# Performance work log

Hardware: AMD Instinct MI355X
Metric: run time of the kernel (lower is better)

The kernel has to match this reference:

```python
import jax, jax.numpy as jnp
import numpy as np

N = 100000
E = 3200000
IN_C = 512
HID = 64
LOC = 64
GLOB = 64
OUT_C = 40
K = 10
ALPHA = 0.1


def setup_inputs() -> dict:
    key = jax.random.key(0)
    ks = jax.random.split(key, 10)
    batch_x = jax.random.normal(ks[0], (N, IN_C), dtype=jnp.float32)
    edge_index = jax.random.randint(ks[1], (2, E), 0, N, dtype=jnp.int32)
    glob_emb = jax.random.normal(ks[2], (N, GLOB), dtype=jnp.float32)
    # Linear params (Glorot-ish scale)
    W1 = jax.random.normal(ks[3], (IN_C, HID), dtype=jnp.float32) / np.sqrt(IN_C)
    b1 = jnp.zeros((HID,), dtype=jnp.float32)
    W2 = jax.random.normal(ks[4], (HID, LOC), dtype=jnp.float32) / np.sqrt(HID)
    b2 = jnp.zeros((LOC,), dtype=jnp.float32)
    # GPR-GNN PPR init coefficients: temp[k] = alpha*(1-alpha)^k, temp[K] = (1-alpha)^K
    temp_np = ALPHA * (1.0 - ALPHA) ** np.arange(K + 1)
    temp_np[-1] = (1.0 - ALPHA) ** K
    temp = jnp.asarray(temp_np, dtype=jnp.float32)
    Wl = jax.random.normal(ks[5], (LOC + GLOB, OUT_C), dtype=jnp.float32) / np.sqrt(LOC + GLOB)
    bl = jnp.zeros((OUT_C,), dtype=jnp.float32)
    return {"batch_x": batch_x, "edge_index": edge_index, "glob_emb": glob_emb,
            "W1": W1, "b1": b1, "W2": W2, "b2": b2, "temp": temp, "Wl": Wl, "bl": bl}


def _gcn_norm(edge_index, num_nodes):
    # add self loops (weight 1), symmetric normalization like PyG gcn_norm
    loops = jnp.arange(num_nodes, dtype=edge_index.dtype)
    row = jnp.concatenate([edge_index[0], loops])  # sources
    col = jnp.concatenate([edge_index[1], loops])  # targets
    w = jnp.ones(row.shape[0], dtype=jnp.float32)
    deg = jax.ops.segment_sum(w, col, num_segments=num_nodes)
    dinv = jnp.where(deg > 0, jax.lax.rsqrt(jnp.maximum(deg, 1.0)), 0.0)
    norm = dinv[row] * dinv[col]
    return row, col, norm


def reference(batch_x, edge_index, glob_emb, W1, b1, W2, b2, temp, Wl, bl):
    # eval mode: all dropouts are identity
    x = jax.nn.relu(batch_x @ W1 + b1)
    x = x @ W2 + b2  # [N, LOC]
    n = x.shape[0]
    row, col, norm = _gcn_norm(edge_index, n)
    hidden = x * temp[0]
    for k in range(K):
        # message: norm * x[src]; aggregate: scatter-add at target
        x = jax.ops.segment_sum(norm[:, None] * x[row], col, num_segments=n)
        hidden = hidden + temp[k + 1] * x
    emb = jnp.concatenate([hidden, glob_emb], axis=1)  # [N, LOC+GLOB]
    return emb @ Wl + bl
```

## Files before the change

### kernel.cpp

```cpp
#include <hip/hip_runtime.h>


typedef _Float16 half8 __attribute__((ext_vector_type(8)));


__global__ __launch_bounds__(256) void count_kernel(const int* __restrict__ edge,
                                                    int* __restrict__ counts, int E) {
  int e = blockIdx.x * 256 + threadIdx.x;
  if (e < E) atomicAdd(&counts[edge[E + e]], 1);
}

__global__ __launch_bounds__(256) void bucketA_kernel(const int* __restrict__ edge,
                                                      unsigned long long* __restrict__ barr,
                                                      int* __restrict__ bcnt,
                                                      int E, int cap) {
  __shared__ int lcnt[64];
  __shared__ int lbase[64];
  int t = threadIdx.x;
  if (t < 64) lcnt[t] = 0;
  __syncthreads();
  int e0 = blockIdx.x * 2048 + t;
  int rk[8];
  int bk[8];
  unsigned long long pk[8];
#pragma unroll
  for (int i = 0; i < 8; ++i) {
    int e = e0 + i * 256;
    int s = 0, c = 0;
    if (e < E) { s = edge[e]; c = edge[E + e]; }
    int b = c >> 11;
    bk[i] = b;
    pk[i] = ((unsigned long long)(unsigned)c << 32) | (unsigned)s;
    if (e < E) rk[i] = atomicAdd(&lcnt[b], 1);
    else rk[i] = -1;
  }
  __syncthreads();
  if (t < 64 && lcnt[t] > 0) lbase[t] = atomicAdd(&bcnt[t], lcnt[t]);
  __syncthreads();
#pragma unroll
  for (int i = 0; i < 8; ++i)
    if (rk[i] >= 0)
      barr[(size_t)bk[i] * cap + lbase[bk[i]] + rk[i]] = pk[i];
}

__global__ __launch_bounds__(256) void fillB_kernel(const unsigned long long* __restrict__ barr,
                                                    const int* __restrict__ bcnt,
                                                    const int* __restrict__ rowptr,
                                                    int* __restrict__ cursor,
                                                    int* __restrict__ srcoff,
                                                    int cap, int nb, int nbx, int cpb) {
  int i = blockIdx.x;
  int x = i & 7;
  int j = i >> 3;
  int bslot = j % nbx;
  int chunk = j / nbx;
  int b = x + 8 * bslot;
  if (b >= nb) return;
  int cnt = bcnt[b];
  int lo = (int)((long long)cnt * chunk / cpb);
  int hi = (int)((long long)cnt * (chunk + 1) / cpb);
  const unsigned long long* ep = barr + (size_t)b * cap;
  for (int e = lo + threadIdx.x; e < hi; e += 256) {
    unsigned long long pk = ep[e];
    int s = (int)(unsigned)pk;
    int c = (int)(pk >> 32);
    int p = rowptr[c] + atomicAdd(&cursor[c], 1);
    srcoff[p] = s * 128;
  }
}

__global__ __launch_bounds__(256) void scanA_kernel(const int* __restrict__ counts,
                                                    int* __restrict__ incl,
                                                    int* __restrict__ partials, int Nn) {
  __shared__ int sbuf[256];
  int t = threadIdx.x;
  int base = blockIdx.x * 1024 + t * 4;
  int a0 = (base + 0 < Nn) ? counts[base + 0] : 0;
  int a1 = (base + 1 < Nn) ? counts[base + 1] : 0;
  int a2 = (base + 2 < Nn) ? counts[base + 2] : 0;
  int a3 = (base + 3 < Nn) ? counts[base + 3] : 0;
  int tot = a0 + a1 + a2 + a3;
  sbuf[t] = tot;
  __syncthreads();
  for (int off = 1; off < 256; off <<= 1) {
    int v = (t >= off) ? sbuf[t - off] : 0;
    __syncthreads();
    sbuf[t] += v;
    __syncthreads();
  }
  int excl = sbuf[t] - tot;
  if (base + 0 < Nn) incl[base + 0] = excl + a0;
  if (base + 1 < Nn) incl[base + 1] = excl + a0 + a1;
  if (base + 2 < Nn) incl[base + 2] = excl + a0 + a1 + a2;
  if (base + 3 < Nn) incl[base + 3] = excl + tot;
  if (t == 255) partials[blockIdx.x] = sbuf[255];
}

__global__ void scanB_kernel(const int* __restrict__ partials,
                             int* __restrict__ chunkoff, int B) {
  __shared__ int sbuf[256];
  int t = threadIdx.x;
  int v = (t < B) ? partials[t] : 0;
  sbuf[t] = v;
  __syncthreads();
  for (int off = 1; off < 256; off <<= 1) {
    int u = (t >= off) ? sbuf[t - off] : 0;
    __syncthreads();
    sbuf[t] += u;
    __syncthreads();
  }
  chunkoff[t] = sbuf[t] - v;
}

__global__ __launch_bounds__(256) void finalize_scan_kernel(const int* __restrict__ incl,
                                                            const int* __restrict__ chunkoff,
                                                            int* __restrict__ rowptr, int Nn) {
  int i = blockIdx.x * 256 + threadIdx.x;
  if (i < Nn) rowptr[i + 1] = incl[i] + chunkoff[i >> 10];
  if (i == 0) rowptr[0] = 0;
}

__global__ __launch_bounds__(256) void dinv_kernel(const int* __restrict__ counts,
                                                   float* __restrict__ dinv, int Nn) {
  int i = blockIdx.x * 256 + threadIdx.x;
  if (i < Nn) dinv[i] = rsqrtf((float)(counts[i] + 1));
}


__global__ __launch_bounds__(256) void mlp1_kernel(const float* __restrict__ X,
                                                   const float* __restrict__ W1,
                                                   const float* __restrict__ b1,
                                                   float* __restrict__ H, int Nn) {
  __shared__ float sXT[64][68];
  __shared__ float sW[64][68];
  int t = threadIdx.x;
  int m0 = blockIdx.x * 64;
  int tx = t & 15, ty = t >> 4;
  float acc[4][4];
#pragma unroll
  for (int i = 0; i < 4; ++i)
#pragma unroll
    for (int j = 0; j < 4; ++j) acc[i][j] = 0.f;

  for (int k0 = 0; k0 < 512; k0 += 64) {
#pragma unroll
    for (int i = 0; i < 4; ++i) {
      int lin = t + i * 256;
      int m = lin >> 4;
      int kq = lin & 15;
      int gr = m0 + m;
      float4 v = make_float4(0.f, 0.f, 0.f, 0.f);
      if (gr < Nn) v = *(const float4*)&X[(size_t)gr * 512 + k0 + kq * 4];
      sXT[kq * 4 + 0][m] = v.x;
      sXT[kq * 4 + 1][m] = v.y;
      sXT[kq * 4 + 2][m] = v.z;
      sXT[kq * 4 + 3][m] = v.w;
    }
#pragma unroll
    for (int i = 0; i < 4; ++i) {
      int lin = t + i * 256;
      int k = lin >> 4;
      int nq = lin & 15;
      float4 v = *(const float4*)&W1[(size_t)(k0 + k) * 64 + nq * 4];
      *(float4*)&sW[k][nq * 4] = v;
    }
    __syncthreads();
#pragma unroll 8
    for (int kk = 0; kk < 64; ++kk) {
      float4 a = *(const float4*)&sXT[kk][ty * 4];
      float4 b = *(const float4*)&sW[kk][tx * 4];
      float av[4] = {a.x, a.y, a.z, a.w};
      float bv[4] = {b.x, b.y, b.z, b.w};
#pragma unroll
      for (int i = 0; i < 4; ++i)
#pragma unroll
        for (int j = 0; j < 4; ++j) acc[i][j] += av[i] * bv[j];
    }
    __syncthreads();
  }
  float4 bb = *(const float4*)&b1[tx * 4];
  float bvv[4] = {bb.x, bb.y, bb.z, bb.w};
#pragma unroll
  for (int i = 0; i < 4; ++i) {
    int r = m0 + ty * 4 + i;
    if (r < Nn) {
      float4 o;
      o.x = fmaxf(acc[i][0] + bvv[0], 0.f);
      o.y = fmaxf(acc[i][1] + bvv[1], 0.f);
      o.z = fmaxf(acc[i][2] + bvv[2], 0.f);
      o.w = fmaxf(acc[i][3] + bvv[3], 0.f);
      *(float4*)&H[(size_t)r * 64 + tx * 4] = o;
    }
  }
}


__global__ void computeM_kernel(const float* __restrict__ W2, const float* __restrict__ Wl,
                                const float* __restrict__ b2, float* __restrict__ Mm,
                                float* __restrict__ cv) {
  int t = threadIdx.x;
  for (int idx = t; idx < 2560; idx += 256) {
    int k = idx / 40, o = idx - k * 40;
    float s = 0.f;
    for (int j = 0; j < 64; ++j) s += W2[k * 64 + j] * Wl[j * 40 + o];
    Mm[idx] = s;
  }
  if (t < 40) {
    float s = 0.f;
    for (int j = 0; j < 64; ++j) s += b2[j] * Wl[j * 40 + t];
    cv[t] = s;
  }
}

__global__ void zeropad_kernel(char* __restrict__ yA, char* __restrict__ yB, int Nn) {
  int t = threadIdx.x;
  ((_Float16*)(yA + (size_t)Nn * 128))[t] = (_Float16)0.f;
  ((_Float16*)(yB + (size_t)Nn * 128))[t] = (_Float16)0.f;
}


__global__ __launch_bounds__(256) void z0_kernel(const float* __restrict__ H,
                                                 const float* __restrict__ Mm,
                                                 const float* __restrict__ cv,
                                                 const float* __restrict__ dinv,
                                                 const float* __restrict__ temp,
                                                 char* __restrict__ y0,
                                                 float* __restrict__ hid, int Nn) {
  __shared__ float sM[2624];
  __shared__ float sc[40];
  int t = threadIdx.x;
  for (int i = t; i < 2560; i += 256) sM[i] = Mm[i];
  for (int i = 2560 + t; i < 2624; i += 256) sM[i] = 0.f;
  if (t < 40) sc[t] = cv[t];
  __syncthreads();
  int wid = t >> 6, lane = t & 63;
  int node = blockIdx.x * 4 + wid;
  if (node < Nn) {
    float h = H[(size_t)node * 64 + lane];
    float acc = (lane < 40) ? sc[lane] : 0.f;
#pragma unroll 8
    for (int k = 0; k < 64; ++k) acc += __shfl(h, k) * sM[k * 40 + lane];
    if (lane < 40) {
      float di = dinv[node];
      float y = di * acc;
      ((_Float16*)(y0 + (size_t)node * 128))[lane] = (_Float16)y;
      hid[(size_t)node * 40 + lane] = temp[0] * y;
    }
  }
}


__global__ __launch_bounds__(256) void prop_kernel(const char* __restrict__ yin,
                                                   char* __restrict__ yout,
                                                   float* __restrict__ hid,
                                                   const int* __restrict__ srcoff,
                                                   const int* __restrict__ rowptr,
                                                   const float* __restrict__ dinv,
                                                   const float* __restrict__ temp,
                                                   int kidx, int Nn) {
  __shared__ float red[4][60][8];
  int t = threadIdx.x, wid = t >> 6, lane = t & 63;
  int node = blockIdx.x * 4 + wid;
  int sub = lane / 5;
  int cl = lane - sub * 5;
  const int zoff = Nn * 128;
  float a0 = 0.f, a1 = 0.f, a2 = 0.f, a3 = 0.f, a4 = 0.f, a5 = 0.f, a6 = 0.f, a7 = 0.f;
  if (node < Nn) {
    int start = rowptr[node], end = rowptr[node + 1];
    int claneoff = cl << 4;
    for (int b0 = start; b0 < end; b0 += 60) {
      int j = b0 + lane;
      int moff = (lane < 60 && j < end) ? srcoff[j] : zoff;
#pragma unroll
      for (int tt = 0; tt < 5; ++tt) {
        int off = __shfl(moff, tt * 12 + sub);
        half8 v = *(const half8*)(yin + off + claneoff);
        a0 += (float)v[0]; a1 += (float)v[1]; a2 += (float)v[2]; a3 += (float)v[3];
        a4 += (float)v[4]; a5 += (float)v[5]; a6 += (float)v[6]; a7 += (float)v[7];
      }
    }
  }
  if (lane < 60) {
    red[wid][lane][0] = a0; red[wid][lane][1] = a1;
    red[wid][lane][2] = a2; red[wid][lane][3] = a3;
    red[wid][lane][4] = a4; red[wid][lane][5] = a5;
    red[wid][lane][6] = a6; red[wid][lane][7] = a7;
  }
  __syncthreads();
  if (node < Nn && lane < 5) {
    float s[8];
#pragma unroll
    for (int i = 0; i < 8; ++i) s[i] = 0.f;
#pragma unroll
    for (int g = 0; g < 12; ++g)
#pragma unroll
      for (int i = 0; i < 8; ++i) s[i] += red[wid][g * 5 + lane][i];
    float di = dinv[node];
    float m = di * di;
    half8 self = *(const half8*)(yin + (size_t)node * 128 + (lane << 4));
    float yn[8];
    half8 outv;
#pragma unroll
    for (int i = 0; i < 8; ++i) {
      yn[i] = m * (s[i] + (float)self[i]);
      outv[i] = (_Float16)yn[i];
    }
    *(half8*)(yout + (size_t)node * 128 + (lane << 4)) = outv;
    float tk = temp[kidx];
    float* hp = &hid[(size_t)node * 40 + lane * 8];
    float4 h0 = *(float4*)hp;
    float4 h1 = *(float4*)(hp + 4);
    h0.x += tk * yn[0]; h0.y += tk * yn[1]; h0.z += tk * yn[2]; h0.w += tk * yn[3];
    h1.x += tk * yn[4]; h1.y += tk * yn[5]; h1.z += tk * yn[6]; h1.w += tk * yn[7];
    *(float4*)hp = h0;
    *(float4*)(hp + 4) = h1;
  }
}


__global__ __launch_bounds__(256) void final_kernel(const float* __restrict__ glob,
                                                    const float* __restrict__ Wl,
                                                    const float* __restrict__ bl,
                                                    const float* __restrict__ hid,
                                                    const int* __restrict__ counts,
                                                    const float* __restrict__ dinv,
                                                    float* __restrict__ out, int Nn) {
  __shared__ float sW[2624];
  __shared__ float sb[40];
  int t = threadIdx.x;
  for (int i = t; i < 2560; i += 256) sW[i] = Wl[2560 + i];
  for (int i = 2560 + t; i < 2624; i += 256) sW[i] = 0.f;
  if (t < 40) sb[t] = bl[t];
  __syncthreads();
  int wid = t >> 6, lane = t & 63;
  int node = blockIdx.x * 4 + wid;
  if (node < Nn) {
    float g = glob[(size_t)node * 64 + lane];
    float acc = (lane < 40) ? sb[lane] : 0.f;
#pragma unroll 8
    for (int k = 0; k < 64; ++k) acc += __shfl(g, k) * sW[k * 40 + lane];
    if (lane < 40) {
      float sc = (float)(counts[node] + 1) * dinv[node];
      out[(size_t)node * 40 + lane] = sc * hid[(size_t)node * 40 + lane] + acc;
    }
  }
}


extern "C" void kernel_launch(void* const* d_in, const int* in_sizes, int n_in,
                              void* d_out, int out_size, void* d_ws, size_t ws_size,
                              hipStream_t stream) {
  const float* X    = (const float*)d_in[0];
  const int*   edge = (const int*)d_in[1];
  const float* glob = (const float*)d_in[2];
  const float* W1   = (const float*)d_in[3];
  const float* b1   = (const float*)d_in[4];
  const float* W2   = (const float*)d_in[5];
  const float* b2   = (const float*)d_in[6];
  const float* temp = (const float*)d_in[7];
  const float* Wl   = (const float*)d_in[8];
  const float* bl   = (const float*)d_in[9];
  float* out = (float*)d_out;

  int Nn = in_sizes[0] / 512;
  int E  = in_sizes[1] / 2;
  int Kk = in_sizes[7] - 1;

  char* p = (char*)d_ws;
  auto alloc = [&](size_t bytes) {
    char* r = p;
    p += (bytes + 255) & ~(size_t)255;
    return r;
  };
  int*   counts   = (int*)alloc((size_t)Nn * 4);
  int*   rowptr   = (int*)alloc((size_t)(Nn + 1) * 4);
  int*   incl     = (int*)alloc((size_t)Nn * 4);
  int*   partials = (int*)alloc(256 * 4);
  int*   chunkoff = (int*)alloc(256 * 4);
  int*   cursor   = (int*)alloc((size_t)Nn * 4);
  float* dinv     = (float*)alloc((size_t)Nn * 4);
  int*   srcoff   = (int*)alloc((size_t)E * 4);
  float* Hbuf     = (float*)alloc((size_t)Nn * 64 * 4);
  float* Mm       = (float*)alloc(2560 * 4);
  float* cv       = (float*)alloc(64 * 4);
  char*  yA       = (char*)alloc((size_t)(Nn + 1) * 128);
  char*  yB       = (char*)alloc((size_t)(Nn + 1) * 128);
  float* hid      = (float*)alloc((size_t)Nn * 40 * 4);

  int nb  = (Nn + 2047) >> 11;
  int nbx = (nb + 7) / 8;
  int cap = E / nb + E / (nb * 8) + 1024;
  unsigned long long* barr = (unsigned long long*)alloc((size_t)nb * cap * 8);
  int* bcnt = (int*)alloc(64 * 4);

  hipMemsetAsync(counts, 0, (size_t)Nn * 4, stream);
  hipMemsetAsync(cursor, 0, (size_t)Nn * 4, stream);
  hipMemsetAsync(bcnt, 0, 64 * 4, stream);

  count_kernel<<<(E + 255) / 256, 256, 0, stream>>>(edge, counts, E);
  bucketA_kernel<<<(E + 2047) / 2048, 256, 0, stream>>>(edge, barr, bcnt, E, cap);
  int B = (Nn + 1023) / 1024;
  scanA_kernel<<<B, 256, 0, stream>>>(counts, incl, partials, Nn);
  scanB_kernel<<<1, 256, 0, stream>>>(partials, chunkoff, B);
  finalize_scan_kernel<<<(Nn + 255) / 256, 256, 0, stream>>>(incl, chunkoff, rowptr, Nn);
  dinv_kernel<<<(Nn + 255) / 256, 256, 0, stream>>>(counts, dinv, Nn);
  int cpb = 32;
  fillB_kernel<<<8 * nbx * cpb, 256, 0, stream>>>(barr, bcnt, rowptr, cursor, srcoff,
                                                  cap, nb, nbx, cpb);

  mlp1_kernel<<<(Nn + 63) / 64, 256, 0, stream>>>(X, W1, b1, Hbuf, Nn);
  computeM_kernel<<<1, 256, 0, stream>>>(W2, Wl, b2, Mm, cv);
  zeropad_kernel<<<1, 64, 0, stream>>>(yA, yB, Nn);

  int nodeBlocks = (Nn + 3) / 4;
  z0_kernel<<<nodeBlocks, 256, 0, stream>>>(Hbuf, Mm, cv, dinv, temp, yA, hid, Nn);

  char* yin = yA;
  char* yout = yB;
  for (int k = 1; k <= Kk; ++k) {
    prop_kernel<<<nodeBlocks, 256, 0, stream>>>(yin, yout, hid, srcoff, rowptr, dinv,
                                                temp, k, Nn);
    char* tmpp = yin; yin = yout; yout = tmpp;
  }

  final_kernel<<<nodeBlocks, 256, 0, stream>>>(glob, Wl, bl, hid, counts, dinv, out, Nn);
}
```

Baseline: 1.415 ms.

## Split fp16 feature rows into 64B+16B planes and use MFMA for first MLP

```diff
diff --git a/kernel.cpp b/kernel.cpp
--- a/kernel.cpp
+++ b/kernel.cpp
@@ -2,6 +2,9 @@
 
 
 typedef _Float16 half8 __attribute__((ext_vector_type(8)));
+typedef _Float16 f16x8 __attribute__((ext_vector_type(8)));
+typedef _Float16 f16x4 __attribute__((ext_vector_type(4)));
+typedef float f32x4 __attribute__((ext_vector_type(4)));
 
 
 __global__ __launch_bounds__(256) void count_kernel(const int* __restrict__ edge,
@@ -65,7 +68,7 @@
     int s = (int)(unsigned)pk;
     int c = (int)(pk >> 32);
     int p = rowptr[c] + atomicAdd(&cursor[c], 1);
-    srcoff[p] = s * 128;
+    srcoff[p] = s;
   }
 }
 
@@ -127,69 +130,69 @@
 }
 
 
-__global__ __launch_bounds__(256) void mlp1_kernel(const float* __restrict__ X,
-                                                   const float* __restrict__ W1,
-                                                   const float* __restrict__ b1,
-                                                   float* __restrict__ H, int Nn) {
-  __shared__ float sXT[64][68];
-  __shared__ float sW[64][68];
+__global__ __launch_bounds__(256) void w1t_kernel(const float* __restrict__ W1,
+                                                  _Float16* __restrict__ W1T) {
+  int idx = blockIdx.x * 256 + threadIdx.x;
+  int col = idx >> 9;
+  int k = idx & 511;
+  W1T[col * 512 + k] = (_Float16)W1[k * 64 + col];
+}
+
+
+__global__ __launch_bounds__(256) void mlp1_mfma_kernel(const float* __restrict__ X,
+                                                        const _Float16* __restrict__ W1T,
+                                                        const float* __restrict__ b1,
+                                                        float* __restrict__ H, int Nn) {
+  __shared__ _Float16 sX[64][88];
+  __shared__ _Float16 sWT[64][88];
   int t = threadIdx.x;
   int m0 = blockIdx.x * 64;
-  int tx = t & 15, ty = t >> 4;
-  float acc[4][4];
-#pragma unroll
-  for (int i = 0; i < 4; ++i)
-#pragma unroll
-    for (int j = 0; j < 4; ++j) acc[i][j] = 0.f;
+  int lane = t & 63, w = t >> 6;
+  f32x4 acc[4];
+#pragma unroll
+  for (int i = 0; i < 4; ++i) acc[i] = (f32x4){0.f, 0.f, 0.f, 0.f};
+  int l15 = lane & 15;
+  int kgrp = (lane >> 4) * 8;
 
   for (int k0 = 0; k0 < 512; k0 += 64) {
 #pragma unroll
     for (int i = 0; i < 4; ++i) {
       int lin = t + i * 256;
       int m = lin >> 4;
-      int kq = lin & 15;
-      int gr = m0 + m;
+      int kq = (lin & 15) * 4;
       float4 v = make_float4(0.f, 0.f, 0.f, 0.f);
-      if (gr < Nn) v = *(const float4*)&X[(size_t)gr * 512 + k0 + kq * 4];
-      sXT[kq * 4 + 0][m] = v.x;
-      sXT[kq * 4 + 1][m] = v.y;
-      sXT[kq * 4 + 2][m] = v.z;
-      sXT[kq * 4 + 3][m] = v.w;
-    }
-#pragma unroll
-    for (int i = 0; i < 4; ++i) {
-      int lin = t + i * 256;
-      int k = lin >> 4;
-      int nq = lin & 15;
-      float4 v = *(const float4*)&W1[(size_t)(k0 + k) * 64 + nq * 4];
-      *(float4*)&sW[k][nq * 4] = v;
-    }
-    __syncthreads();
-#pragma unroll 8
-    for (int kk = 0; kk < 64; ++kk) {
-      float4 a = *(const float4*)&sXT[kk][ty * 4];
-      float4 b = *(const float4*)&sW[kk][tx * 4];
-      float av[4] = {a.x, a.y, a.z, a.w};
-      float bv[4] = {b.x, b.y, b.z, b.w};
-#pragma unroll
-      for (int i = 0; i < 4; ++i)
-#pragma unroll
-        for (int j = 0; j < 4; ++j) acc[i][j] += av[i] * bv[j];
-    }
-    __syncthreads();
-  }
-  float4 bb = *(const float4*)&b1[tx * 4];
-  float bvv[4] = {bb.x, bb.y, bb.z, bb.w};
-#pragma unroll
-  for (int i = 0; i < 4; ++i) {
-    int r = m0 + ty * 4 + i;
-    if (r < Nn) {
-      float4 o;
-      o.x = fmaxf(acc[i][0] + bvv[0], 0.f);
-      o.y = fmaxf(acc[i][1] + bvv[1], 0.f);
-      o.z = fmaxf(acc[i][2] + bvv[2], 0.f);
-      o.w = fmaxf(acc[i][3] + bvv[3], 0.f);
-      *(float4*)&H[(size_t)r * 64 + tx * 4] = o;
+      if (m0 + m < Nn) v = *(const float4*)&X[(size_t)(m0 + m) * 512 + k0 + kq];
+      f16x4 h4 = {(_Float16)v.x, (_Float16)v.y, (_Float16)v.z, (_Float16)v.w};
+      *(f16x4*)&sX[m][kq] = h4;
+    }
+#pragma unroll
+    for (int i = 0; i < 2; ++i) {
+      int c = t + i * 256;
+      int col = c >> 3;
+      int k8 = (c & 7) * 8;
+      f16x8 v = *(const f16x8*)&W1T[col * 512 + k0 + k8];
+      *(f16x8*)&sWT[col][k8] = v;
+    }
+    __syncthreads();
+#pragma unroll
+    for (int kc = 0; kc < 2; ++kc) {
+      f16x8 a = *(const f16x8*)&sX[16 * w + l15][kc * 32 + kgrp];
+#pragma unroll
+      for (int c = 0; c < 4; ++c) {
+        f16x8 b = *(const f16x8*)&sWT[c * 16 + l15][kc * 32 + kgrp];
+        acc[c] = __builtin_amdgcn_mfma_f32_16x16x32_f16(a, b, acc[c], 0, 0, 0);
+      }
+    }
+    __syncthreads();
+  }
+  int rbase = m0 + 16 * w + (lane >> 4) * 4;
+#pragma unroll
+  for (int c = 0; c < 4; ++c) {
+    float bias = b1[c * 16 + l15];
+#pragma unroll
+    for (int r = 0; r < 4; ++r) {
+      int row = rbase + r;
+      if (row < Nn) H[(size_t)row * 64 + c * 16 + l15] = fmaxf(acc[c][r] + bias, 0.f);
     }
   }
 }
@@ -212,10 +215,16 @@
   }
 }
 
-__global__ void zeropad_kernel(char* __restrict__ yA, char* __restrict__ yB, int Nn) {
-  int t = threadIdx.x;
-  ((_Float16*)(yA + (size_t)Nn * 128))[t] = (_Float16)0.f;
-  ((_Float16*)(yB + (size_t)Nn * 128))[t] = (_Float16)0.f;
+__global__ void zeropad_kernel(char* __restrict__ yA, char* __restrict__ yB,
+                               int Nn, int yboff) {
+  int t = threadIdx.x;
+  if (t < 32) {
+    ((_Float16*)(yA + (size_t)Nn * 64))[t] = (_Float16)0.f;
+    ((_Float16*)(yB + (size_t)Nn * 64))[t] = (_Float16)0.f;
+  } else if (t < 40) {
+    ((_Float16*)(yA + yboff + (size_t)Nn * 16))[t - 32] = (_Float16)0.f;
+    ((_Float16*)(yB + yboff + (size_t)Nn * 16))[t - 32] = (_Float16)0.f;
+  }
 }
 
 
@@ -225,7 +234,7 @@
                                                  const float* __restrict__ dinv,
                                                  const float* __restrict__ temp,
                                                  char* __restrict__ y0,
-                                                 float* __restrict__ hid, int Nn) {
+                                                 float* __restrict__ hid, int Nn, int yboff) {
   __shared__ float sM[2624];
   __shared__ float sc[40];
   int t = threadIdx.x;
@@ -243,7 +252,10 @@
     if (lane < 40) {
       float di = dinv[node];
       float y = di * acc;
-      ((_Float16*)(y0 + (size_t)node * 128))[lane] = (_Float16)y;
+      if (lane < 32)
+        ((_Float16*)(y0 + (size_t)node * 64))[lane] = (_Float16)y;
+      else
+        ((_Float16*)(y0 + yboff + (size_t)node * 16))[lane - 32] = (_Float16)y;
       hid[(size_t)node * 40 + lane] = temp[0] * y;
     }
   }
@@ -257,24 +269,24 @@
                                                    const int* __restrict__ rowptr,
                                                    const float* __restrict__ dinv,
                                                    const float* __restrict__ temp,
-                                                   int kidx, int Nn) {
+                                                   int kidx, int Nn, int yboff) {
   __shared__ float red[4][60][8];
   int t = threadIdx.x, wid = t >> 6, lane = t & 63;
   int node = blockIdx.x * 4 + wid;
   int sub = lane / 5;
   int cl = lane - sub * 5;
-  const int zoff = Nn * 128;
+  int lmul = (cl == 4) ? 16 : 64;
+  int ladd = (cl == 4) ? yboff : (cl << 4);
   float a0 = 0.f, a1 = 0.f, a2 = 0.f, a3 = 0.f, a4 = 0.f, a5 = 0.f, a6 = 0.f, a7 = 0.f;
   if (node < Nn) {
     int start = rowptr[node], end = rowptr[node + 1];
-    int claneoff = cl << 4;
     for (int b0 = start; b0 < end; b0 += 60) {
       int j = b0 + lane;
-      int moff = (lane < 60 && j < end) ? srcoff[j] : zoff;
+      int msrc = (lane < 60 && j < end) ? srcoff[j] : Nn;
 #pragma unroll
       for (int tt = 0; tt < 5; ++tt) {
-        int off = __shfl(moff, tt * 12 + sub);
-        half8 v = *(const half8*)(yin + off + claneoff);
+        int n = __shfl(msrc, tt * 12 + sub);
+        half8 v = *(const half8*)(yin + (size_t)(n * lmul + ladd));
         a0 += (float)v[0]; a1 += (float)v[1]; a2 += (float)v[2]; a3 += (float)v[3];
         a4 += (float)v[4]; a5 += (float)v[5]; a6 += (float)v[6]; a7 += (float)v[7];
       }
@@ -297,7 +309,9 @@
       for (int i = 0; i < 8; ++i) s[i] += red[wid][g * 5 + lane][i];
     float di = dinv[node];
     float m = di * di;
-    half8 self = *(const half8*)(yin + (size_t)node * 128 + (lane << 4));
+    int lm2 = (lane == 4) ? 16 : 64;
+    int la2 = (lane == 4) ? yboff : (lane << 4);
+    half8 self = *(const half8*)(yin + (size_t)(node * lm2 + la2));
     float yn[8];
     half8 outv;
 #pragma unroll
@@ -305,7 +319,7 @@
       yn[i] = m * (s[i] + (float)self[i]);
       outv[i] = (_Float16)yn[i];
     }
-    *(half8*)(yout + (size_t)node * 128 + (lane << 4)) = outv;
+    *(half8*)(yout + (size_t)(node * lm2 + la2)) = outv;
     float tk = temp[kidx];
     float* hp = &hid[(size_t)node * 40 + lane * 8];
     float4 h0 = *(float4*)hp;
@@ -383,8 +397,11 @@
   float* Hbuf     = (float*)alloc((size_t)Nn * 64 * 4);
   float* Mm       = (float*)alloc(2560 * 4);
   float* cv       = (float*)alloc(64 * 4);
-  char*  yA       = (char*)alloc((size_t)(Nn + 1) * 128);
-  char*  yB       = (char*)alloc((size_t)(Nn + 1) * 128);
+  _Float16* W1T   = (_Float16*)alloc(64 * 512 * 2);
+  int yboff = (Nn + 1) * 64;
+  size_t ybytes = (size_t)(Nn + 1) * 80;
+  char*  yA       = (char*)alloc(ybytes);
+  char*  yB       = (char*)alloc(ybytes);
   float* hid      = (float*)alloc((size_t)Nn * 40 * 4);
 
   int nb  = (Nn + 2047) >> 11;
@@ -408,18 +425,19 @@
   fillB_kernel<<<8 * nbx * cpb, 256, 0, stream>>>(barr, bcnt, rowptr, cursor, srcoff,
                                                   cap, nb, nbx, cpb);
 
-  mlp1_kernel<<<(Nn + 63) / 64, 256, 0, stream>>>(X, W1, b1, Hbuf, Nn);
+  w1t_kernel<<<128, 256, 0, stream>>>(W1, W1T);
+  mlp1_mfma_kernel<<<(Nn + 63) / 64, 256, 0, stream>>>(X, W1T, b1, Hbuf, Nn);
   computeM_kernel<<<1, 256, 0, stream>>>(W2, Wl, b2, Mm, cv);
-  zeropad_kernel<<<1, 64, 0, stream>>>(yA, yB, Nn);
+  zeropad_kernel<<<1, 64, 0, stream>>>(yA, yB, Nn, yboff);
 
   int nodeBlocks = (Nn + 3) / 4;
-  z0_kernel<<<nodeBlocks, 256, 0, stream>>>(Hbuf, Mm, cv, dinv, temp, yA, hid, Nn);
+  z0_kernel<<<nodeBlocks, 256, 0, stream>>>(Hbuf, Mm, cv, dinv, temp, yA, hid, Nn, yboff);
 
   char* yin = yA;
   char* yout = yB;
   for (int k = 1; k <= Kk; ++k) {
     prop_kernel<<<nodeBlocks, 256, 0, stream>>>(yin, yout, hid, srcoff, rowptr, dinv,
-                                                temp, k, Nn);
+                                                temp, k, Nn, yboff);
     char* tmpp = yin; yin = yout; yout = tmpp;
   }
 
```

Result: slower. 1.454 ms (+2.8%).
